# Kernel optimization log

Measured on AMD Instinct MI355X. Metric: run time of the kernel, lower is better.

The kernel has to match this reference:

```python
import jax, jax.numpy as jnp
import numpy as np

N_NODES = 50000
N_EDGES = 800000
IN_DIM = 128
HEADS = 8
F_OUT = 16


def setup_inputs() -> dict:
    key = jax.random.key(0)
    ks = jax.random.split(key, 7)
    x = jax.random.normal(ks[0], (N_NODES, IN_DIM), dtype=jnp.float32)
    edge_index = jax.random.randint(ks[1], (2, N_EDGES), 0, N_NODES, dtype=jnp.int32)
    # xavier-normal-ish scale
    W_proj = jax.random.normal(ks[2], (HEADS * F_OUT, IN_DIM), dtype=jnp.float32) * (2.0 / (IN_DIM + HEADS * F_OUT)) ** 0.5
    a_src = jax.random.normal(ks[3], (HEADS, F_OUT), dtype=jnp.float32) * 0.1
    a_tgt = jax.random.normal(ks[4], (HEADS, F_OUT), dtype=jnp.float32) * 0.1
    W_skip = jax.random.normal(ks[5], (HEADS * F_OUT, IN_DIM), dtype=jnp.float32) * (2.0 / (IN_DIM + HEADS * F_OUT)) ** 0.5
    bias = jnp.zeros((HEADS * F_OUT,), dtype=jnp.float32)
    return {"x": x, "edge_index": edge_index, "W_proj": W_proj, "a_src": a_src,
            "a_tgt": a_tgt, "W_skip": W_skip, "bias": bias}


def reference(x, edge_index, W_proj, a_src, a_tgt, W_skip, bias):
    N = x.shape[0]
    src, tgt = edge_index[0], edge_index[1]
    # project: [N, H, F]
    proj = (x @ W_proj.T).reshape(N, HEADS, F_OUT)
    # per-node partial scores: [N, H]
    s_src = jnp.einsum('nhf,hf->nh', proj, a_src)
    s_tgt = jnp.einsum('nhf,hf->nh', proj, a_tgt)
    # per-edge scores, LeakyReLU(0.2): [E, H]
    e = jax.nn.leaky_relu(s_src[src] + s_tgt[tgt], negative_slope=0.2)
    # segment softmax over incoming edges of each target node
    e_max = jax.ops.segment_max(e, tgt, num_segments=N)
    e_exp = jnp.exp(e - e_max[tgt])
    denom = jax.ops.segment_sum(e_exp, tgt, num_segments=N)
    alpha = e_exp / (denom[tgt] + 1e-16)  # [E, H]
    # weighted scatter-add of projected source features: [N, H, F]
    msgs = proj[src] * alpha[:, :, None]
    out = jax.ops.segment_sum(msgs, tgt, num_segments=N)
    # skip connection (in_dim != out_dim path -> skip_proj), concat heads, bias, ELU
    out = out + (x @ W_skip.T).reshape(N, HEADS, F_OUT)
    out = out.reshape(N, HEADS * F_OUT) + bias
    return jax.nn.elu(out)
```

## Files before the change

kernel.cpp:

```cpp
#include <hip/hip_runtime.h>
#include <hip/hip_bf16.h>
#include <math.h>

#define PADN 50048
#define CAP 64

typedef __attribute__((ext_vector_type(8))) short short8;
typedef __attribute__((ext_vector_type(4))) float f32x4;

__device__ __forceinline__ unsigned short f2b(float f) {
  __hip_bfloat16 h = __float2bfloat16(f);
  return *(unsigned short*)&h;
}

__global__ __launch_bounds__(256) void k_init(const float* __restrict__ Wp,
                                              const float* __restrict__ Ws,
                                              const float* __restrict__ a_src,
                                              const float* __restrict__ a_tgt,
                                              unsigned short* __restrict__ Bpk,
                                              int* __restrict__ counts,
                                              int N, int zeroB) {
  const int b = blockIdx.x;
  if (b < zeroB) {
    int i = b * 256 + threadIdx.x;
    if (i < N) counts[i] = 0;
    return;
  }
  int idx = (b - zeroB) * 256 + threadIdx.x;
  int tile = idx >> 8;
  int ks = (idx >> 6) & 3;
  int lane = idx & 63;
  int kbase = ks * 32 + (lane >> 4) * 8;
  unsigned short o[8];
  if (tile < 16) {
    int col = tile * 16 + (lane & 15);
    const float* src = (col < 128) ? (Wp + (size_t)col * 128 + kbase)
                                   : (Ws + (size_t)(col - 128) * 128 + kbase);
#pragma unroll
    for (int j = 0; j < 8; ++j) o[j] = f2b(src[j]);
  } else {
    int col = lane & 15;
    int h = col & 7;
    const float* av = (col < 8) ? (a_src + h * 16) : (a_tgt + h * 16);
#pragma unroll
    for (int j = 0; j < 8; ++j) {
      int k = kbase + j;
      float s = 0.f;
#pragma unroll
      for (int f = 0; f < 16; ++f) s = fmaf(Wp[(size_t)(h * 16 + f) * 128 + k], av[f], s);
      o[j] = f2b(s);
    }
  }
  *(short8*)(Bpk + (size_t)idx * 8) = *(short8*)o;
}

__global__ __launch_bounds__(256) void k_cg(
    const float* __restrict__ x, const unsigned short* __restrict__ Bpk,
    unsigned short* __restrict__ pb, unsigned short* __restrict__ sb,
    float* __restrict__ ssrc, float* __restrict__ stgt,
    const int* __restrict__ ei, int* __restrict__ counts,
    int* __restrict__ esrc, int N, int E, int cntB) {
  const int b = blockIdx.x;
  if (b < cntB) {
    const int tid = b * 256 + threadIdx.x;
    const int T = cntB * 256;
    const int* srcp = ei;
    const int* tgtp = ei + E;
    int e[8], s[8], t[8], r[8];
#pragma unroll
    for (int p = 0; p < 8; ++p) {
      e[p] = tid + p * T;
      t[p] = (e[p] < E) ? tgtp[e[p]] : 0;
      s[p] = (e[p] < E) ? srcp[e[p]] : 0;
    }
#pragma unroll
    for (int p = 0; p < 8; ++p)
      r[p] = (e[p] < E) ? atomicAdd(&counts[t[p]], 1) : CAP;
#pragma unroll
    for (int p = 0; p < 8; ++p)
      if (r[p] < CAP && e[p] < E) esrc[(t[p] << 6) + r[p]] = s[p];
    return;
  }

  const int wave = threadIdx.x >> 6, lane = threadIdx.x & 63;
  const int m = lane & 15, q = lane >> 4;
  const int r0 = (b - cntB) * 64 + wave * 16;
  const int row_a = r0 + m;

  short8 a[4];
#pragma unroll
  for (int ks = 0; ks < 4; ++ks) {
    float4 v0 = make_float4(0.f, 0.f, 0.f, 0.f), v1 = v0;
    if (row_a < N) {
      const float4* xp = (const float4*)(x + (size_t)row_a * 128 + ks * 32 + q * 8);
      v0 = xp[0];
      v1 = xp[1];
    }
    unsigned short o[8];
    o[0] = f2b(v0.x); o[1] = f2b(v0.y); o[2] = f2b(v0.z); o[3] = f2b(v0.w);
    o[4] = f2b(v1.x); o[5] = f2b(v1.y); o[6] = f2b(v1.z); o[7] = f2b(v1.w);
    a[ks] = *(short8*)o;
  }

  for (int ct = 0; ct < 16; ++ct) {
    f32x4 acc = {0.f, 0.f, 0.f, 0.f};
#pragma unroll
    for (int ks = 0; ks < 4; ++ks) {
      short8 bfr = *(const short8*)(Bpk + (size_t)((ct * 4 + ks) * 64 + lane) * 8);
      acc = __builtin_amdgcn_mfma_f32_16x16x32_bf16(a[ks], bfr, acc, 0, 0, 0);
    }
    unsigned short* dst = (ct < 8) ? pb : sb;
    const int cc = (ct & 7) * 16 + m;
#pragma unroll
    for (int r = 0; r < 4; ++r) {
      int row = r0 + q * 4 + r;
      if (row < N) dst[(size_t)row * 128 + cc] = f2b(acc[r]);
    }
  }
  {
    f32x4 acc = {0.f, 0.f, 0.f, 0.f};
#pragma unroll
    for (int ks = 0; ks < 4; ++ks) {
      short8 bfr = *(const short8*)(Bpk + (size_t)((16 * 4 + ks) * 64 + lane) * 8);
      acc = __builtin_amdgcn_mfma_f32_16x16x32_bf16(a[ks], bfr, acc, 0, 0, 0);
    }
    float* sd = (m < 8) ? ssrc : stgt;
    const int h = m & 7;
#pragma unroll
    for (int r = 0; r < 4; ++r) {
      int row = r0 + q * 4 + r;
      if (row < N) sd[row * 8 + h] = acc[r];
    }
  }
}

__global__ __launch_bounds__(256) void k_agg(const unsigned short* __restrict__ pb,
                                             const unsigned short* __restrict__ sb,
                                             const float* __restrict__ ssrc,
                                             const float* __restrict__ stgt,
                                             const float* __restrict__ bias,
                                             const int* __restrict__ counts,
                                             const int* __restrict__ esrc,
                                             float* __restrict__ out, int N) {
  int wid = (int)((blockIdx.x * (size_t)blockDim.x + threadIdx.x) >> 6);
  int lane = threadIdx.x & 63;
  if (wid >= N) return;
  const int n = wid;
  const int c = lane * 2;
  const int h = lane >> 3;

  const float st = stgt[n * 8 + h];
  const int cnt = min(counts[n], CAP);

  float ds0 = 0.f, ds1 = 0.f, ds2 = 0.f, ds3 = 0.f;
  float x00 = 0.f, x01 = 0.f, x10 = 0.f, x11 = 0.f;
  float x20 = 0.f, x21 = 0.f, x30 = 0.f, x31 = 0.f;

#define FILLQ(p, jj)                                              \
  {                                                               \
    int s_ = __builtin_amdgcn_readlane(srcv, (jj));               \
    pv##p = *(const unsigned int*)(pb + (size_t)s_ * 128 + c);    \
    sc##p = ssrc[s_ * 8 + h];                                     \
  }
#define EDGEQ(p, dsx, a0x, a1x)                                   \
  {                                                               \
    float e_ = sc##p + st;                                        \
    e_ = fmaxf(e_, 0.2f * e_);                                    \
    float w_ = __expf(e_);                                        \
    dsx += w_;                                                    \
    a0x = fmaf(w_, __uint_as_float(pv##p << 16), a0x);            \
    a1x = fmaf(w_, __uint_as_float(pv##p & 0xffff0000u), a1x);    \
  }

  if (cnt > 0) {
    const int cm = cnt - 1;
    int srcv = esrc[(n << 6) + min(lane, cm)];
    unsigned int pv0, pv1, pv2, pv3, pv4, pv5, pv6, pv7;
    float sc0, sc1, sc2, sc3, sc4, sc5, sc6, sc7;

    FILLQ(0, 0)
    FILLQ(1, min(1, cm))
    FILLQ(2, min(2, cm))
    FILLQ(3, min(3, cm))
    FILLQ(4, min(4, cm))
    FILLQ(5, min(5, cm))
    FILLQ(6, min(6, cm))
    FILLQ(7, min(7, cm))

    int j = 0;
    for (; j + 8 <= cnt; j += 8) {
      EDGEQ(0, ds0, x00, x01)
      EDGEQ(1, ds1, x10, x11)
      EDGEQ(2, ds2, x20, x21)
      EDGEQ(3, ds3, x30, x31)
      if (j + 8 < cnt) {
        FILLQ(0, min(j + 8, cm))
        FILLQ(1, min(j + 9, cm))
        FILLQ(2, min(j + 10, cm))
        FILLQ(3, min(j + 11, cm))
      }
      EDGEQ(4, ds0, x00, x01)
      EDGEQ(5, ds1, x10, x11)
      EDGEQ(6, ds2, x20, x21)
      EDGEQ(7, ds3, x30, x31)
      if (j + 12 < cnt) {
        FILLQ(4, min(j + 12, cm))
        FILLQ(5, min(j + 13, cm))
        FILLQ(6, min(j + 14, cm))
        FILLQ(7, min(j + 15, cm))
      }
    }
    const int rem = cnt - j;
    if (rem > 0) EDGEQ(0, ds0, x00, x01)
    if (rem > 1) EDGEQ(1, ds1, x10, x11)
    if (rem > 2) EDGEQ(2, ds2, x20, x21)
    if (rem > 3) EDGEQ(3, ds3, x30, x31)
    if (rem > 4) EDGEQ(4, ds0, x00, x01)
    if (rem > 5) EDGEQ(5, ds1, x10, x11)
    if (rem > 6) EDGEQ(6, ds2, x20, x21)
  }
#undef FILLQ
#undef EDGEQ

  const float dsum = (ds0 + ds1) + (ds2 + ds3);
  const float acc0 = (x00 + x10) + (x20 + x30);
  const float acc1 = (x01 + x11) + (x21 + x31);
  const float inv = 1.0f / (dsum + 1e-16f);
  size_t row = (size_t)n * 128;
  unsigned int su = *(const unsigned int*)(sb + row + c);
  float sk0 = __uint_as_float(su << 16);
  float sk1 = __uint_as_float(su & 0xffff0000u);
  float r0 = fmaf(acc0, inv, sk0) + bias[c];
  float r1 = fmaf(acc1, inv, sk1) + bias[c + 1];
  r0 = (r0 > 0.f) ? r0 : (__expf(r0) - 1.0f);
  r1 = (r1 > 0.f) ? r1 : (__expf(r1) - 1.0f);
  *(float2*)(out + row + c) = make_float2(r0, r1);
}

extern "C" void kernel_launch(void* const* d_in, const int* in_sizes, int n_in,
                              void* d_out, int out_size, void* d_ws, size_t ws_size,
                              hipStream_t stream) {
  const float* x = (const float*)d_in[0];
  const int* ei = (const int*)d_in[1];
  const float* Wp = (const float*)d_in[2];
  const float* a_src = (const float*)d_in[3];
  const float* a_tgt = (const float*)d_in[4];
  const float* Ws = (const float*)d_in[5];
  const float* bias = (const float*)d_in[6];
  float* out = (float*)d_out;

  const int N = in_sizes[0] / 128;
  const int E = in_sizes[1] / 2;

  unsigned short* Bpk = (unsigned short*)d_ws;
  unsigned short* pb = Bpk + 34816;
  unsigned short* sb = pb + (size_t)N * 128;
  float* ssrc = (float*)(sb + (size_t)N * 128);
  float* stgt = ssrc + (size_t)N * 8;
  int* counts = (int*)(stgt + (size_t)N * 8);
  int* esrc = counts + N;

  const int zeroB = (N + 255) / 256;
  const int cntB = (E + 8 * 256 - 1) / (8 * 256);
  const int gemmB = PADN / 64;

  k_init<<<zeroB + 17, 256, 0, stream>>>(Wp, Ws, a_src, a_tgt, Bpk, counts, N, zeroB);
  k_cg<<<cntB + gemmB, 256, 0, stream>>>(x, Bpk, pb, sb, ssrc, stgt, ei, counts,
                                         esrc, N, E, cntB);
  k_agg<<<(N + 3) / 4, 256, 0, stream>>>(pb, sb, ssrc, stgt, bias, counts, esrc, out, N);
}
```

Before: 184.1 us.

## Process two row tiles per wave and double-buffer B fragments in projection GEMM

Each wave in the projection GEMM now handles 32 rows instead of 16, so every loaded B fragment feeds two MFMAs. B fragments for the next column tile are prefetched into a double buffer while the current tile computes, and the score column tile is folded into the same fully unrolled loop. This halves the number of GEMM blocks and cuts redundant B loads, at the cost of more registers per thread and possibly lower occupancy.

```diff
diff --git a/kernel.cpp b/kernel.cpp
--- a/kernel.cpp
+++ b/kernel.cpp
@@ -84,54 +84,71 @@
 
   const int wave = threadIdx.x >> 6, lane = threadIdx.x & 63;
   const int m = lane & 15, q = lane >> 4;
-  const int r0 = (b - cntB) * 64 + wave * 16;
-  const int row_a = r0 + m;
-
-  short8 a[4];
-#pragma unroll
-  for (int ks = 0; ks < 4; ++ks) {
-    float4 v0 = make_float4(0.f, 0.f, 0.f, 0.f), v1 = v0;
-    if (row_a < N) {
-      const float4* xp = (const float4*)(x + (size_t)row_a * 128 + ks * 32 + q * 8);
-      v0 = xp[0];
-      v1 = xp[1];
-    }
-    unsigned short o[8];
-    o[0] = f2b(v0.x); o[1] = f2b(v0.y); o[2] = f2b(v0.z); o[3] = f2b(v0.w);
-    o[4] = f2b(v1.x); o[5] = f2b(v1.y); o[6] = f2b(v1.z); o[7] = f2b(v1.w);
-    a[ks] = *(short8*)o;
-  }
-
-  for (int ct = 0; ct < 16; ++ct) {
-    f32x4 acc = {0.f, 0.f, 0.f, 0.f};
+  const int r0 = (b - cntB) * 128 + wave * 32;
+
+  short8 a[2][4];
+#pragma unroll
+  for (int g = 0; g < 2; ++g) {
+    const int row_a = r0 + g * 16 + m;
 #pragma unroll
     for (int ks = 0; ks < 4; ++ks) {
-      short8 bfr = *(const short8*)(Bpk + (size_t)((ct * 4 + ks) * 64 + lane) * 8);
-      acc = __builtin_amdgcn_mfma_f32_16x16x32_bf16(a[ks], bfr, acc, 0, 0, 0);
-    }
-    unsigned short* dst = (ct < 8) ? pb : sb;
-    const int cc = (ct & 7) * 16 + m;
-#pragma unroll
-    for (int r = 0; r < 4; ++r) {
-      int row = r0 + q * 4 + r;
-      if (row < N) dst[(size_t)row * 128 + cc] = f2b(acc[r]);
-    }
-  }
-  {
-    f32x4 acc = {0.f, 0.f, 0.f, 0.f};
+      float4 v0 = make_float4(0.f, 0.f, 0.f, 0.f), v1 = v0;
+      if (row_a < N) {
+        const float4* xp = (const float4*)(x + (size_t)row_a * 128 + ks * 32 + q * 8);
+        v0 = xp[0];
+        v1 = xp[1];
+      }
+      unsigned short o[8];
+      o[0] = f2b(v0.x); o[1] = f2b(v0.y); o[2] = f2b(v0.z); o[3] = f2b(v0.w);
+      o[4] = f2b(v1.x); o[5] = f2b(v1.y); o[6] = f2b(v1.z); o[7] = f2b(v1.w);
+      a[g][ks] = *(short8*)o;
+    }
+  }
+
+#define LOADB(dst, t)                                                        \
+  {                                                                          \
+    const unsigned short* bp_ = Bpk + (size_t)((t) * 256 + lane) * 8;        \
+    dst[0] = *(const short8*)(bp_ + 0 * 512);                                \
+    dst[1] = *(const short8*)(bp_ + 1 * 512);                                \
+    dst[2] = *(const short8*)(bp_ + 2 * 512);                                \
+    dst[3] = *(const short8*)(bp_ + 3 * 512);                                \
+  }
+
+  short8 bb[2][4];
+  LOADB(bb[0], 0)
+#pragma unroll
+  for (int ct = 0; ct < 17; ++ct) {
+    if (ct < 16) LOADB(bb[(ct + 1) & 1], ct + 1)
+    f32x4 acc0 = {0.f, 0.f, 0.f, 0.f};
+    f32x4 acc1 = {0.f, 0.f, 0.f, 0.f};
 #pragma unroll
     for (int ks = 0; ks < 4; ++ks) {
-      short8 bfr = *(const short8*)(Bpk + (size_t)((16 * 4 + ks) * 64 + lane) * 8);
-      acc = __builtin_amdgcn_mfma_f32_16x16x32_bf16(a[ks], bfr, acc, 0, 0, 0);
-    }
-    float* sd = (m < 8) ? ssrc : stgt;
-    const int h = m & 7;
-#pragma unroll
-    for (int r = 0; r < 4; ++r) {
-      int row = r0 + q * 4 + r;
-      if (row < N) sd[row * 8 + h] = acc[r];
-    }
-  }
+      acc0 = __builtin_amdgcn_mfma_f32_16x16x32_bf16(a[0][ks], bb[ct & 1][ks], acc0, 0, 0, 0);
+      acc1 = __builtin_amdgcn_mfma_f32_16x16x32_bf16(a[1][ks], bb[ct & 1][ks], acc1, 0, 0, 0);
+    }
+    if (ct < 16) {
+      unsigned short* dst = (ct < 8) ? pb : sb;
+      const int cc = (ct & 7) * 16 + m;
+#pragma unroll
+      for (int r = 0; r < 4; ++r) {
+        int row0 = r0 + q * 4 + r;
+        if (row0 < N) dst[(size_t)row0 * 128 + cc] = f2b(acc0[r]);
+        int row1 = r0 + 16 + q * 4 + r;
+        if (row1 < N) dst[(size_t)row1 * 128 + cc] = f2b(acc1[r]);
+      }
+    } else {
+      float* sd = (m < 8) ? ssrc : stgt;
+      const int h = m & 7;
+#pragma unroll
+      for (int r = 0; r < 4; ++r) {
+        int row0 = r0 + q * 4 + r;
+        if (row0 < N) sd[row0 * 8 + h] = acc0[r];
+        int row1 = r0 + 16 + q * 4 + r;
+        if (row1 < N) sd[row1 * 8 + h] = acc1[r];
+      }
+    }
+  }
+#undef LOADB
 }
 
 __global__ __launch_bounds__(256) void k_agg(const unsigned short* __restrict__ pb,
@@ -262,7 +279,7 @@
 
   const int zeroB = (N + 255) / 256;
   const int cntB = (E + 8 * 256 - 1) / (8 * 256);
-  const int gemmB = PADN / 64;
+  const int gemmB = PADN / 128;
 
   k_init<<<zeroB + 17, 256, 0, stream>>>(Wp, Ws, a_src, a_tgt, Bpk, counts, N, zeroB);
   k_cg<<<cntB + gemmB, 256, 0, stream>>>(x, Bpk, pb, sb, ssrc, stgt, ei, counts,
```

After: 184.7 us. Within noise of the previous version (+0.3%).
